# Performance work log

Hardware: AMD Instinct MI355X
Metric: run time of the kernel (lower is better)

Reference implementation:

```python
import jax, jax.numpy as jnp
import numpy as np

N_TOKENS = 4096   # flattened batch*seq tokens
D_MODEL = 1024
N_EXPERT = 8
D_HIDDEN = 1024   # expert FFN hidden size
TOP_K = 2


def setup_inputs() -> dict:
    key = jax.random.key(0)
    ks = jax.random.split(key, 4)
    f32 = jnp.float32
    return {
        "inp": jax.random.normal(ks[0], (N_TOKENS, D_MODEL), f32),
        "gate_w": jax.random.normal(ks[1], (D_MODEL, N_EXPERT), f32) * 0.02,
        "gate_b": jnp.zeros((N_EXPERT,), f32),
        "w1": jax.random.normal(ks[2], (N_EXPERT, D_MODEL, D_HIDDEN), f32) * 0.02,
        "b1": jnp.zeros((N_EXPERT, D_HIDDEN), f32),
        "w2": jax.random.normal(ks[3], (N_EXPERT, D_HIDDEN, D_MODEL), f32) * 0.02,
        "b2": jnp.zeros((N_EXPERT, D_MODEL), f32),
    }


def reference(inp, gate_w, gate_b, w1, b1, w2, b2):
    """FMoE forward: NaiveGate top-k -> dispatch -> per-expert FFN -> weighted combine.

    Math is identical to dispatch/grouped-GEMM/gather: since both top-k slots of a
    token see the same input, out[n] = sum_e coeff[n,e] * expert_e(inp[n]) where
    coeff[n,e] = sum_k softmax(top_vals)[n,k] * 1[top_idx[n,k] == e].
    """
    n_expert = gate_w.shape[-1]
    # NaiveGate: linear gate, top-k, softmax over the k selected logits
    logits = inp @ gate_w + gate_b                      # [N, E]
    top_val, top_idx = jax.lax.top_k(logits, TOP_K)     # [N, K]
    score = jax.nn.softmax(top_val, axis=-1)            # [N, K]
    # combine weights per (token, expert); top-k indices are distinct per token
    coeff = jnp.sum(
        jax.nn.one_hot(top_idx, n_expert, dtype=inp.dtype) * score[..., None],
        axis=1,
    )                                                   # [N, E]
    # expert FFN (exact-erf GeLU, matching torch.nn.functional.gelu)
    h = jax.nn.gelu(jnp.einsum('nd,edh->neh', inp, w1) + b1, approximate=False)  # [N, E, H]
    out = jnp.einsum('neh,ehd->nd', h * coeff[:, :, None], w2) + coeff @ b2      # [N, D]
    return out


if __name__ == "__main__":
    out = reference(**setup_inputs())
    print(out.shape, out.dtype)
```

## Files before the change

kernel.cpp:

```cpp
#include <hip/hip_runtime.h>
#include <math.h>

#define N_TOKENS 4096
#define D_MODEL  1024
#define N_EXPERT 8
#define D_HIDDEN 1024
#define N_POS    8192

typedef __bf16 bf16x8 __attribute__((ext_vector_type(8)));
typedef float  f32x4  __attribute__((ext_vector_type(4)));
typedef unsigned short u16x8 __attribute__((ext_vector_type(8)));

#define GLOBAL_AS __attribute__((address_space(1)))
#define LDS_AS    __attribute__((address_space(3)))

static __device__ __forceinline__ void async_ld16(const void* g, void* l) {
    __builtin_amdgcn_global_load_lds((GLOBAL_AS void*)g, (LDS_AS void*)l, 16, 0, 0);
}

static __device__ __forceinline__ unsigned short f2bf(float f) {
    unsigned int u = __builtin_bit_cast(unsigned int, f);
    u += 0x7fffu + ((u >> 16) & 1u);
    return (unsigned short)(u >> 16);
}
static __device__ __forceinline__ unsigned int pack2(float a, float b) {
    return (unsigned int)f2bf(a) | ((unsigned int)f2bf(b) << 16);
}
static __device__ __forceinline__ float bflo(unsigned int u) {
    return __builtin_bit_cast(float, u << 16);
}
static __device__ __forceinline__ float bfhi(unsigned int u) {
    return __builtin_bit_cast(float, u & 0xffff0000u);
}

__global__ __launch_bounds__(256) void convert_kernel(
    const float* __restrict__ w1, const float* __restrict__ w2,
    const float* __restrict__ inp,
    unsigned short* __restrict__ w1b, unsigned short* __restrict__ w2b,
    unsigned short* __restrict__ inp_bf, int* __restrict__ cnts)
{
    int tid = threadIdx.x;
    if (blockIdx.x == 0 && blockIdx.y == 0 && blockIdx.z == 0 && tid < 8)
        cnts[tid] = 0;
    int mat = blockIdx.z;
    int r0 = blockIdx.x * 64, c0 = blockIdx.y * 64;

    if (mat >= 16) {
        const float* src = inp + (size_t)(mat - 16) * 1048576;
        unsigned short* dst = inp_bf + (size_t)(mat - 16) * 1048576;
        #pragma unroll
        for (int i = 0; i < 4; ++i) {
            int r = (tid >> 4) + i * 16;
            float4 v = *(const float4*)(src + (size_t)(r0 + r) * 1024 + c0 + (tid & 15) * 4);
            uint2 u; u.x = pack2(v.x, v.y); u.y = pack2(v.z, v.w);
            *(uint2*)(dst + (size_t)(r0 + r) * 1024 + c0 + (tid & 15) * 4) = u;
        }
        return;
    }

    const float* src = (mat < 8) ? (w1 + (size_t)mat * 1048576)
                                 : (w2 + (size_t)(mat - 8) * 1048576);
    unsigned short* dst = (mat < 8) ? (w1b + (size_t)mat * 1048576)
                                    : (w2b + (size_t)(mat - 8) * 1048576);
    __shared__ float tile[64][68];
    #pragma unroll
    for (int i = 0; i < 4; ++i) {
        int r = (tid >> 4) + i * 16;
        float4 v = *(const float4*)(src + (size_t)(r0 + r) * 1024 + c0 + (tid & 15) * 4);
        *(float4*)&tile[r][(tid & 15) * 4] = v;
    }
    __syncthreads();
    int dr = tid >> 2;
    #pragma unroll
    for (int p = 0; p < 2; ++p) {
        int ch = (tid & 3) + p * 4;
        u16x8 o;
        #pragma unroll
        for (int j = 0; j < 8; ++j) o[j] = f2bf(tile[ch * 8 + j][dr]);
        *(u16x8*)(dst + (size_t)(c0 + dr) * 1024 + r0 + ch * 8) = o;
    }
}

__global__ __launch_bounds__(256) void gate_kernel(
    const float* __restrict__ inp, const float* __restrict__ gate_w,
    const float* __restrict__ gate_b, int* __restrict__ cnts,
    int* __restrict__ emeta, float* __restrict__ stok)
{
    __shared__ int bcnt[8], base[8];
    __shared__ int tinfo[16];
    int tid = threadIdx.x, lane = tid & 63, wave = tid >> 6;
    if (tid < 8) bcnt[tid] = 0;
    __syncthreads();

    for (int t = 0; t < 4; ++t) {
        int ti = wave * 4 + t;
        int n  = blockIdx.x * 16 + ti;
        const float* ip = inp + (size_t)n * D_MODEL;
        float acc[8] = {0.f,0.f,0.f,0.f,0.f,0.f,0.f,0.f};
        for (int d0 = lane * 4; d0 < D_MODEL; d0 += 256) {
            float4 x = *(const float4*)(ip + d0);
            #pragma unroll
            for (int j = 0; j < 4; ++j) {
                float xv = (j == 0) ? x.x : (j == 1) ? x.y : (j == 2) ? x.z : x.w;
                float4 g0 = *(const float4*)(gate_w + (d0 + j) * 8);
                float4 g1 = *(const float4*)(gate_w + (d0 + j) * 8 + 4);
                acc[0] += xv * g0.x; acc[1] += xv * g0.y;
                acc[2] += xv * g0.z; acc[3] += xv * g0.w;
                acc[4] += xv * g1.x; acc[5] += xv * g1.y;
                acc[6] += xv * g1.z; acc[7] += xv * g1.w;
            }
        }
        #pragma unroll
        for (int off = 32; off > 0; off >>= 1)
            #pragma unroll
            for (int e = 0; e < 8; ++e)
                acc[e] += __shfl_xor(acc[e], off, 64);
        #pragma unroll
        for (int e = 0; e < 8; ++e) acc[e] += gate_b[e];

        int e0 = 0; float v0 = acc[0];
        #pragma unroll
        for (int e = 1; e < 8; ++e) if (acc[e] > v0) { v0 = acc[e]; e0 = e; }
        int e1 = -1; float v1 = -1e30f;
        #pragma unroll
        for (int e = 0; e < 8; ++e) if (e != e0 && acc[e] > v1) { v1 = acc[e]; e1 = e; }
        float tv = expf(v1 - v0);
        float s0 = 1.0f / (1.0f + tv);
        float s1 = tv / (1.0f + tv);

        if (lane == 0) {
            int r0 = atomicAdd(&bcnt[e0], 1);
            int r1 = atomicAdd(&bcnt[e1], 1);
            tinfo[ti] = e0 | (e1 << 4) | (r0 << 8) | (r1 << 20);
            stok[2 * n]     = s0;
            stok[2 * n + 1] = s1;
        }
    }
    __syncthreads();
    if (tid < 8) base[tid] = atomicAdd(&cnts[tid], bcnt[tid]);
    __syncthreads();
    if (tid < 16) {
        int n = blockIdx.x * 16 + tid;
        unsigned int inf = (unsigned int)tinfo[tid];
        int e0 = inf & 15, e1 = (inf >> 4) & 15;
        int p0 = base[e0] + ((inf >> 8) & 4095);
        int p1 = base[e1] + (int)(inf >> 20);
        emeta[n] = e0 | (e1 << 4) | (p0 << 8) | (p1 << 20);
    }
}

__global__ __launch_bounds__(256) void plan_kernel(
    const int* __restrict__ cnts, const int* __restrict__ emeta,
    int* __restrict__ pos2tok)
{
    int n = blockIdx.x * 256 + threadIdx.x;
    unsigned int em = (unsigned int)emeta[n];
    int e0 = em & 15, e1 = (em >> 4) & 15;
    int p0 = (em >> 8) & 4095, p1 = (int)(em >> 20);
    int off0 = 0, off1 = 0;
    #pragma unroll
    for (int e = 0; e < 8; ++e) {
        int c = cnts[e];
        off0 += (e < e0) ? c : 0;
        off1 += (e < e1) ? c : 0;
    }
    pos2tok[off0 + p0] = n;
    pos2tok[off1 + p1] = n;
}

__global__ __launch_bounds__(256, 4) void ffn1_kernel(
    const unsigned short* __restrict__ inp_bf, const unsigned short* __restrict__ w1b,
    const float* __restrict__ b1, const int* __restrict__ cnts,
    const int* __restrict__ pos2tok, unsigned short* __restrict__ Hg)
{
    int bid = blockIdx.x;
    int e = bid & 7, nt = (bid >> 3) & 15, mt = bid >> 7;
    int off = 0, Ne = 0;
    #pragma unroll
    for (int i = 0; i < 8; ++i) {
        int c = cnts[i];
        off += (i < e) ? c : 0;
        Ne = (i == e) ? c : Ne;
    }
    int m0 = mt * 128;
    if (m0 >= Ne) return;
    int n0 = nt * 64;

    __shared__ unsigned short As[2 * 128 * 32];
    __shared__ unsigned short Bs[2 * 64 * 32];
    __shared__ int rowtok[128];

    int tid = threadIdx.x, lane = tid & 63, wave = tid >> 6;
    int lrow = lane >> 2, lchunk = lane & 3;
    int csw8 = (lchunk ^ ((lrow >> 1) & 3)) * 8;

    if (tid < 128) {
        int r = m0 + tid;
        if (r >= Ne) r = Ne - 1;
        rowtok[tid] = pos2tok[off + r];
    }
    __syncthreads();

    const unsigned short* aS0 =
        inp_bf + (size_t)rowtok[wave * 32 + lrow] * D_MODEL + csw8;
    const unsigned short* aS1 =
        inp_bf + (size_t)rowtok[wave * 32 + 16 + lrow] * D_MODEL + csw8;
    const unsigned short* bS = w1b + (size_t)e * D_MODEL * D_HIDDEN
                             + (size_t)(n0 + wave * 16 + lrow) * D_MODEL + csw8;
    unsigned short* aD0 = &As[(wave * 32) * 32];
    unsigned short* aD1 = &As[(wave * 32 + 16) * 32];
    unsigned short* bD  = &Bs[(wave * 16) * 32];

    f32x4 acc[4][2] = {};
    int wm = (wave & 1) * 64, wn = ((wave >> 1) & 1) * 32;
    int lane15 = lane & 15, quad = lane >> 4;
    int fro = (quad ^ ((lane15 >> 1) & 3)) * 8;

    for (int k0 = 0; k0 < D_MODEL; k0 += 64) {
        #pragma unroll
        for (int h = 0; h < 2; ++h) {
            int ko = k0 + h * 32;
            async_ld16(aS0 + ko, aD0 + h * 4096);
            async_ld16(aS1 + ko, aD1 + h * 4096);
            async_ld16(bS  + ko, bD  + h * 2048);
        }
        __syncthreads();
        #pragma unroll
        for (int h = 0; h < 2; ++h) {
            bf16x8 af[4], bf[2];
            #pragma unroll
            for (int t = 0; t < 4; ++t)
                af[t] = *(const bf16x8*)&As[h * 4096 + (wm + t * 16 + lane15) * 32 + fro];
            #pragma unroll
            for (int t = 0; t < 2; ++t)
                bf[t] = *(const bf16x8*)&Bs[h * 2048 + (wn + t * 16 + lane15) * 32 + fro];
            #pragma unroll
            for (int i = 0; i < 4; ++i)
                #pragma unroll
                for (int j = 0; j < 2; ++j)
                    acc[i][j] = __builtin_amdgcn_mfma_f32_16x16x32_bf16(
                        af[i], bf[j], acc[i][j], 0, 0, 0);
        }
        if (k0 + 64 < D_MODEL) __syncthreads();
    }

    const float* bexp = b1 + (size_t)e * D_HIDDEN;
    #pragma unroll
    for (int j = 0; j < 2; ++j) {
        int gcol = n0 + wn + j * 16 + lane15;
        float bv = bexp[gcol];
        #pragma unroll
        for (int i = 0; i < 4; ++i) {
            int rowb = wm + i * 16 + quad * 4;
            #pragma unroll
            for (int r = 0; r < 4; ++r) {
                int row = rowb + r;
                if (m0 + row < Ne) {
                    float x = acc[i][j][r] + bv;
                    float gv = 0.5f * x * (1.0f + erff(x * 0.70710678118654752f));
                    Hg[(size_t)(off + m0 + row) * D_HIDDEN + gcol] = f2bf(gv);
                }
            }
        }
    }
}

__global__ __launch_bounds__(256, 4) void ffn2_kernel(
    const unsigned short* __restrict__ Hg, const unsigned short* __restrict__ w2b,
    const int* __restrict__ cnts, unsigned short* __restrict__ Og)
{
    int bid = blockIdx.x;
    int e = bid & 7, nt = (bid >> 3) & 15, mt = bid >> 7;
    int off = 0, Ne = 0;
    #pragma unroll
    for (int i = 0; i < 8; ++i) {
        int c = cnts[i];
        off += (i < e) ? c : 0;
        Ne = (i == e) ? c : Ne;
    }
    int m0 = mt * 128;
    if (m0 >= Ne) return;
    int n0 = nt * 64;

    __shared__ unsigned short As[2 * 128 * 32];
    __shared__ unsigned short Bs[2 * 64 * 32];

    int tid = threadIdx.x, lane = tid & 63, wave = tid >> 6;
    int lrow = lane >> 2, lchunk = lane & 3;
    int csw8 = (lchunk ^ ((lrow >> 1) & 3)) * 8;

    int ga0 = off + m0 + wave * 32 + lrow;
    int ga1 = ga0 + 16;
    if (ga0 >= N_POS) ga0 = N_POS - 1;
    if (ga1 >= N_POS) ga1 = N_POS - 1;
    const unsigned short* aS0 = Hg + (size_t)ga0 * D_HIDDEN + csw8;
    const unsigned short* aS1 = Hg + (size_t)ga1 * D_HIDDEN + csw8;
    const unsigned short* bS = w2b + (size_t)e * D_HIDDEN * D_MODEL
                             + (size_t)(n0 + wave * 16 + lrow) * D_HIDDEN + csw8;
    unsigned short* aD0 = &As[(wave * 32) * 32];
    unsigned short* aD1 = &As[(wave * 32 + 16) * 32];
    unsigned short* bD  = &Bs[(wave * 16) * 32];

    f32x4 acc[4][2] = {};
    int wm = (wave & 1) * 64, wn = ((wave >> 1) & 1) * 32;
    int lane15 = lane & 15, quad = lane >> 4;
    int fro = (quad ^ ((lane15 >> 1) & 3)) * 8;

    for (int k0 = 0; k0 < D_HIDDEN; k0 += 64) {
        #pragma unroll
        for (int h = 0; h < 2; ++h) {
            int ko = k0 + h * 32;
            async_ld16(aS0 + ko, aD0 + h * 4096);
            async_ld16(aS1 + ko, aD1 + h * 4096);
            async_ld16(bS  + ko, bD  + h * 2048);
        }
        __syncthreads();
        #pragma unroll
        for (int h = 0; h < 2; ++h) {
            bf16x8 af[4], bf[2];
            #pragma unroll
            for (int t = 0; t < 4; ++t)
                af[t] = *(const bf16x8*)&As[h * 4096 + (wm + t * 16 + lane15) * 32 + fro];
            #pragma unroll
            for (int t = 0; t < 2; ++t)
                bf[t] = *(const bf16x8*)&Bs[h * 2048 + (wn + t * 16 + lane15) * 32 + fro];
            #pragma unroll
            for (int i = 0; i < 4; ++i)
                #pragma unroll
                for (int j = 0; j < 2; ++j)
                    acc[i][j] = __builtin_amdgcn_mfma_f32_16x16x32_bf16(
                        af[i], bf[j], acc[i][j], 0, 0, 0);
        }
        if (k0 + 64 < D_HIDDEN) __syncthreads();
    }

    #pragma unroll
    for (int j = 0; j < 2; ++j) {
        int gcol = n0 + wn + j * 16 + lane15;
        #pragma unroll
        for (int i = 0; i < 4; ++i) {
            int rowb = wm + i * 16 + quad * 4;
            #pragma unroll
            for (int r = 0; r < 4; ++r) {
                int row = rowb + r;
                if (m0 + row < Ne) {
                    Og[(size_t)(off + m0 + row) * D_MODEL + gcol] =
                        f2bf(acc[i][j][r]);
                }
            }
        }
    }
}

__global__ __launch_bounds__(256) void combine_kernel(
    const unsigned short* __restrict__ Og, const int* __restrict__ cnts,
    const int* __restrict__ emeta, const float* __restrict__ stok,
    const float* __restrict__ b2, float* __restrict__ out)
{
    int lane = threadIdx.x & 63, wave = threadIdx.x >> 6;
    int n = blockIdx.x * 4 + wave;
    unsigned int em = (unsigned int)emeta[n];
    int e0 = em & 15, e1 = (em >> 4) & 15;
    int p0 = (em >> 8) & 4095, p1 = (int)(em >> 20);
    int off0 = 0, off1 = 0;
    #pragma unroll
    for (int e = 0; e < 8; ++e) {
        int c = cnts[e];
        off0 += (e < e0) ? c : 0;
        off1 += (e < e1) ? c : 0;
    }
    int pos0 = off0 + p0, pos1 = off1 + p1;
    float s0 = stok[2 * n], s1 = stok[2 * n + 1];
    const unsigned short* o0 = Og + (size_t)pos0 * D_MODEL;
    const unsigned short* o1 = Og + (size_t)pos1 * D_MODEL;
    const float* bA = b2 + (size_t)e0 * D_MODEL;
    const float* bB = b2 + (size_t)e1 * D_MODEL;
    float* op = out + (size_t)n * D_MODEL;
    for (int d = lane * 4; d < D_MODEL; d += 256) {
        uint2 u0 = *(const uint2*)(o0 + d);
        uint2 u1 = *(const uint2*)(o1 + d);
        float4 xa = *(const float4*)(bA + d);
        float4 xb = *(const float4*)(bB + d);
        float4 r;
        r.x = s0 * (bflo(u0.x) + xa.x) + s1 * (bflo(u1.x) + xb.x);
        r.y = s0 * (bfhi(u0.x) + xa.y) + s1 * (bfhi(u1.x) + xb.y);
        r.z = s0 * (bflo(u0.y) + xa.z) + s1 * (bflo(u1.y) + xb.z);
        r.w = s0 * (bfhi(u0.y) + xa.w) + s1 * (bfhi(u1.y) + xb.w);
        *(float4*)(op + d) = r;
    }
}

extern "C" void kernel_launch(void* const* d_in, const int* in_sizes, int n_in,
                              void* d_out, int out_size, void* d_ws, size_t ws_size,
                              hipStream_t stream) {
    const float* inp    = (const float*)d_in[0];
    const float* gate_w = (const float*)d_in[1];
    const float* gate_b = (const float*)d_in[2];
    const float* w1     = (const float*)d_in[3];
    const float* b1     = (const float*)d_in[4];
    const float* w2     = (const float*)d_in[5];
    const float* b2     = (const float*)d_in[6];
    float* out = (float*)d_out;

    char* ws = (char*)d_ws;
    int*   cnts    = (int*)  (ws);
    int*   emeta   = (int*)  (ws + 4096);
    float* stok    = (float*)(ws + 65536);
    int*   pos2tok = (int*)  (ws + 131072);
    unsigned short* w2b = (unsigned short*)(ws + 1048576);
    unsigned short* Hg  = (unsigned short*)(ws + 17825792);
    unsigned short* w1b = (unsigned short*)(ws + 34603008);
    unsigned short* Og  = (unsigned short*)(ws + 34603008);

    unsigned short* inp_bf = (unsigned short*)d_out;

    convert_kernel<<<dim3(16, 16, 20), 256, 0, stream>>>(
        w1, w2, inp, w1b, w2b, inp_bf, cnts);
    gate_kernel<<<dim3(N_TOKENS / 16), 256, 0, stream>>>(
        inp, gate_w, gate_b, cnts, emeta, stok);
    plan_kernel<<<dim3(N_TOKENS / 256), 256, 0, stream>>>(cnts, emeta, pos2tok);
    ffn1_kernel<<<dim3(4096), 256, 0, stream>>>(
        inp_bf, w1b, b1, cnts, pos2tok, Hg);
    ffn2_kernel<<<dim3(4096), 256, 0, stream>>>(Hg, w2b, cnts, Og);
    combine_kernel<<<dim3(N_TOKENS / 4), 256, 0, stream>>>(
        Og, cnts, emeta, stok, b2, out);
}
```

Measured before the change: 224.5 us.

## Fuse MoE pipeline into one persistent cooperative kernel with grid syncs

Replaces the six separate launches (convert, gate, plan, ffn1, ffn2, combine) with a single cooperative kernel of 512 persistent blocks that loops over work items and separates stages with grid-wide syncs. Expert counting no longer uses global atomics: per-group counts are written out and one block computes the prefix offsets, a token-to-position map and the position-to-token map. The aim is to remove per-launch overhead and inter-kernel gaps. In exchange, occupancy is capped at two blocks per CU (down from four in the GEMM kernels), which may hurt latency hiding in the expert GEMMs, and the single-block planning step adds a serial phase.

```diff
diff --git a/kernel.cpp b/kernel.cpp
--- a/kernel.cpp
+++ b/kernel.cpp
@@ -1,5 +1,8 @@
 #include <hip/hip_runtime.h>
+#include <hip/hip_cooperative_groups.h>
 #include <math.h>
+
+namespace cg = cooperative_groups;
 
 #define N_TOKENS 4096
 #define D_MODEL  1024
@@ -33,360 +36,356 @@
     return __builtin_bit_cast(float, u & 0xffff0000u);
 }
 
-__global__ __launch_bounds__(256) void convert_kernel(
-    const float* __restrict__ w1, const float* __restrict__ w2,
-    const float* __restrict__ inp,
+__global__ __launch_bounds__(256, 2) void moe_kernel(
+    const float* __restrict__ inp, const float* __restrict__ gate_w,
+    const float* __restrict__ gate_b, const float* __restrict__ w1,
+    const float* __restrict__ b1, const float* __restrict__ w2,
+    const float* __restrict__ b2,
     unsigned short* __restrict__ w1b, unsigned short* __restrict__ w2b,
-    unsigned short* __restrict__ inp_bf, int* __restrict__ cnts)
+    unsigned short* __restrict__ inp_bf, unsigned short* __restrict__ Hg,
+    unsigned short* __restrict__ Og,
+    int* __restrict__ gcnt, int* __restrict__ emeta, float* __restrict__ stok,
+    int* __restrict__ pos2tok, int* __restrict__ tok2pos,
+    int* __restrict__ cnts, float* __restrict__ out)
 {
-    int tid = threadIdx.x;
-    if (blockIdx.x == 0 && blockIdx.y == 0 && blockIdx.z == 0 && tid < 8)
-        cnts[tid] = 0;
-    int mat = blockIdx.z;
-    int r0 = blockIdx.x * 64, c0 = blockIdx.y * 64;
-
-    if (mat >= 16) {
-        const float* src = inp + (size_t)(mat - 16) * 1048576;
-        unsigned short* dst = inp_bf + (size_t)(mat - 16) * 1048576;
-        #pragma unroll
-        for (int i = 0; i < 4; ++i) {
-            int r = (tid >> 4) + i * 16;
-            float4 v = *(const float4*)(src + (size_t)(r0 + r) * 1024 + c0 + (tid & 15) * 4);
-            uint2 u; u.x = pack2(v.x, v.y); u.y = pack2(v.z, v.w);
-            *(uint2*)(dst + (size_t)(r0 + r) * 1024 + c0 + (tid & 15) * 4) = u;
-        }
-        return;
+    cg::grid_group grid = cg::this_grid();
+    __shared__ __align__(16) char smem[25088];
+
+    int bid = blockIdx.x, tid = threadIdx.x;
+    int lane = tid & 63, wave = tid >> 6;
+    int lane15 = lane & 15, quad = lane >> 4;
+
+    for (int job = bid; job < 5376; job += 512) {
+        if (job < 5120) {
+            int mat = job >> 8, t = job & 255;
+            int r0 = (t & 15) * 64, c0 = (t >> 4) * 64;
+            if (mat >= 16) {
+                const float* src = inp + (size_t)(mat - 16) * 1048576;
+                unsigned short* dst = inp_bf + (size_t)(mat - 16) * 1048576;
+                #pragma unroll
+                for (int i = 0; i < 4; ++i) {
+                    int r = (tid >> 4) + i * 16;
+                    float4 v = *(const float4*)(src + (size_t)(r0 + r) * 1024
+                                                + c0 + (tid & 15) * 4);
+                    uint2 u; u.x = pack2(v.x, v.y); u.y = pack2(v.z, v.w);
+                    *(uint2*)(dst + (size_t)(r0 + r) * 1024 + c0 + (tid & 15) * 4) = u;
+                }
+            } else {
+                const float* src = (mat < 8) ? (w1 + (size_t)mat * 1048576)
+                                             : (w2 + (size_t)(mat - 8) * 1048576);
+                unsigned short* dst = (mat < 8) ? (w1b + (size_t)mat * 1048576)
+                                                : (w2b + (size_t)(mat - 8) * 1048576);
+                float (*tile)[68] = (float(*)[68])smem;
+                #pragma unroll
+                for (int i = 0; i < 4; ++i) {
+                    int r = (tid >> 4) + i * 16;
+                    float4 v = *(const float4*)(src + (size_t)(r0 + r) * 1024
+                                                + c0 + (tid & 15) * 4);
+                    *(float4*)&tile[r][(tid & 15) * 4] = v;
+                }
+                __syncthreads();
+                int dr = tid >> 2;
+                #pragma unroll
+                for (int p = 0; p < 2; ++p) {
+                    int ch = (tid & 3) + p * 4;
+                    u16x8 o;
+                    #pragma unroll
+                    for (int j = 0; j < 8; ++j) o[j] = f2bf(tile[ch * 8 + j][dr]);
+                    *(u16x8*)(dst + (size_t)(c0 + dr) * 1024 + r0 + ch * 8) = o;
+                }
+            }
+        } else {
+            int g = job - 5120;
+            int* bcnt  = (int*)smem;
+            int* tinfo = bcnt + 8;
+            if (tid < 8) bcnt[tid] = 0;
+            __syncthreads();
+            for (int t = 0; t < 4; ++t) {
+                int ti = wave * 4 + t;
+                int n  = g * 16 + ti;
+                const float* ip = inp + (size_t)n * D_MODEL;
+                float acc[8] = {0.f,0.f,0.f,0.f,0.f,0.f,0.f,0.f};
+                for (int d0 = lane * 4; d0 < D_MODEL; d0 += 256) {
+                    float4 x = *(const float4*)(ip + d0);
+                    #pragma unroll
+                    for (int j = 0; j < 4; ++j) {
+                        float xv = (j == 0) ? x.x : (j == 1) ? x.y
+                                 : (j == 2) ? x.z : x.w;
+                        float4 g0 = *(const float4*)(gate_w + (d0 + j) * 8);
+                        float4 g1 = *(const float4*)(gate_w + (d0 + j) * 8 + 4);
+                        acc[0] += xv * g0.x; acc[1] += xv * g0.y;
+                        acc[2] += xv * g0.z; acc[3] += xv * g0.w;
+                        acc[4] += xv * g1.x; acc[5] += xv * g1.y;
+                        acc[6] += xv * g1.z; acc[7] += xv * g1.w;
+                    }
+                }
+                #pragma unroll
+                for (int off = 32; off > 0; off >>= 1)
+                    #pragma unroll
+                    for (int e = 0; e < 8; ++e)
+                        acc[e] += __shfl_xor(acc[e], off, 64);
+                #pragma unroll
+                for (int e = 0; e < 8; ++e) acc[e] += gate_b[e];
+
+                int e0 = 0; float v0 = acc[0];
+                #pragma unroll
+                for (int e = 1; e < 8; ++e) if (acc[e] > v0) { v0 = acc[e]; e0 = e; }
+                int e1 = -1; float v1 = -1e30f;
+                #pragma unroll
+                for (int e = 0; e < 8; ++e)
+                    if (e != e0 && acc[e] > v1) { v1 = acc[e]; e1 = e; }
+                float tv = expf(v1 - v0);
+                float s0 = 1.0f / (1.0f + tv);
+                float s1 = tv / (1.0f + tv);
+                if (lane == 0) {
+                    int r0 = atomicAdd(&bcnt[e0], 1);
+                    int r1 = atomicAdd(&bcnt[e1], 1);
+                    tinfo[ti] = e0 | (e1 << 4) | (r0 << 8) | (r1 << 20);
+                    stok[2 * n]     = s0;
+                    stok[2 * n + 1] = s1;
+                }
+            }
+            __syncthreads();
+            if (tid < 8)  gcnt[g * 8 + tid]  = bcnt[tid];
+            if (tid < 16) emeta[g * 16 + tid] = tinfo[tid];
+        }
+        __syncthreads();
     }
-
-    const float* src = (mat < 8) ? (w1 + (size_t)mat * 1048576)
-                                 : (w2 + (size_t)(mat - 8) * 1048576);
-    unsigned short* dst = (mat < 8) ? (w1b + (size_t)mat * 1048576)
-                                    : (w2b + (size_t)(mat - 8) * 1048576);
-    __shared__ float tile[64][68];
-    #pragma unroll
-    for (int i = 0; i < 4; ++i) {
-        int r = (tid >> 4) + i * 16;
-        float4 v = *(const float4*)(src + (size_t)(r0 + r) * 1024 + c0 + (tid & 15) * 4);
-        *(float4*)&tile[r][(tid & 15) * 4] = v;
+    grid.sync();
+
+    if (bid == 0) {
+        int* lc  = (int*)smem;
+        int* lb  = lc + 2048;
+        int* lex = lb + 2048;
+        for (int i = tid; i < 2048; i += 256) lc[i] = gcnt[i];
+        __syncthreads();
+        if (tid < 8) {
+            int run = 0;
+            for (int g = 0; g < 256; ++g) {
+                lb[g * 8 + tid] = run;
+                run += lc[g * 8 + tid];
+            }
+            lex[8 + tid] = run;
+            cnts[tid] = run;
+        }
+        __syncthreads();
+        if (tid == 0) {
+            int o = 0;
+            #pragma unroll
+            for (int e = 0; e < 8; ++e) { lex[e] = o; o += lex[8 + e]; }
+        }
+        __syncthreads();
+        {
+            int g = tid;
+            for (int ti = 0; ti < 16; ++ti) {
+                int n = g * 16 + ti;
+                unsigned int em = (unsigned int)emeta[n];
+                int e0 = em & 15, e1 = (em >> 4) & 15;
+                int r0 = (em >> 8) & 4095, r1 = (int)(em >> 20);
+                int pos0 = lex[e0] + lb[g * 8 + e0] + r0;
+                int pos1 = lex[e1] + lb[g * 8 + e1] + r1;
+                tok2pos[2 * n]     = pos0;
+                tok2pos[2 * n + 1] = pos1;
+                pos2tok[pos0] = n;
+                pos2tok[pos1] = n;
+            }
+        }
     }
-    __syncthreads();
-    int dr = tid >> 2;
-    #pragma unroll
-    for (int p = 0; p < 2; ++p) {
-        int ch = (tid & 3) + p * 4;
-        u16x8 o;
-        #pragma unroll
-        for (int j = 0; j < 8; ++j) o[j] = f2bf(tile[ch * 8 + j][dr]);
-        *(u16x8*)(dst + (size_t)(c0 + dr) * 1024 + r0 + ch * 8) = o;
-    }
-}
-
-__global__ __launch_bounds__(256) void gate_kernel(
-    const float* __restrict__ inp, const float* __restrict__ gate_w,
-    const float* __restrict__ gate_b, int* __restrict__ cnts,
-    int* __restrict__ emeta, float* __restrict__ stok)
-{
-    __shared__ int bcnt[8], base[8];
-    __shared__ int tinfo[16];
-    int tid = threadIdx.x, lane = tid & 63, wave = tid >> 6;
-    if (tid < 8) bcnt[tid] = 0;
-    __syncthreads();
-
-    for (int t = 0; t < 4; ++t) {
-        int ti = wave * 4 + t;
-        int n  = blockIdx.x * 16 + ti;
-        const float* ip = inp + (size_t)n * D_MODEL;
-        float acc[8] = {0.f,0.f,0.f,0.f,0.f,0.f,0.f,0.f};
-        for (int d0 = lane * 4; d0 < D_MODEL; d0 += 256) {
-            float4 x = *(const float4*)(ip + d0);
-            #pragma unroll
-            for (int j = 0; j < 4; ++j) {
-                float xv = (j == 0) ? x.x : (j == 1) ? x.y : (j == 2) ? x.z : x.w;
-                float4 g0 = *(const float4*)(gate_w + (d0 + j) * 8);
-                float4 g1 = *(const float4*)(gate_w + (d0 + j) * 8 + 4);
-                acc[0] += xv * g0.x; acc[1] += xv * g0.y;
-                acc[2] += xv * g0.z; acc[3] += xv * g0.w;
-                acc[4] += xv * g1.x; acc[5] += xv * g1.y;
-                acc[6] += xv * g1.z; acc[7] += xv * g1.w;
-            }
-        }
-        #pragma unroll
-        for (int off = 32; off > 0; off >>= 1)
-            #pragma unroll
-            for (int e = 0; e < 8; ++e)
-                acc[e] += __shfl_xor(acc[e], off, 64);
-        #pragma unroll
-        for (int e = 0; e < 8; ++e) acc[e] += gate_b[e];
-
-        int e0 = 0; float v0 = acc[0];
-        #pragma unroll
-        for (int e = 1; e < 8; ++e) if (acc[e] > v0) { v0 = acc[e]; e0 = e; }
-        int e1 = -1; float v1 = -1e30f;
-        #pragma unroll
-        for (int e = 0; e < 8; ++e) if (e != e0 && acc[e] > v1) { v1 = acc[e]; e1 = e; }
-        float tv = expf(v1 - v0);
-        float s0 = 1.0f / (1.0f + tv);
-        float s1 = tv / (1.0f + tv);
-
-        if (lane == 0) {
-            int r0 = atomicAdd(&bcnt[e0], 1);
-            int r1 = atomicAdd(&bcnt[e1], 1);
-            tinfo[ti] = e0 | (e1 << 4) | (r0 << 8) | (r1 << 20);
-            stok[2 * n]     = s0;
-            stok[2 * n + 1] = s1;
-        }
-    }
-    __syncthreads();
-    if (tid < 8) base[tid] = atomicAdd(&cnts[tid], bcnt[tid]);
-    __syncthreads();
-    if (tid < 16) {
-        int n = blockIdx.x * 16 + tid;
-        unsigned int inf = (unsigned int)tinfo[tid];
-        int e0 = inf & 15, e1 = (inf >> 4) & 15;
-        int p0 = base[e0] + ((inf >> 8) & 4095);
-        int p1 = base[e1] + (int)(inf >> 20);
-        emeta[n] = e0 | (e1 << 4) | (p0 << 8) | (p1 << 20);
-    }
-}
-
-__global__ __launch_bounds__(256) void plan_kernel(
-    const int* __restrict__ cnts, const int* __restrict__ emeta,
-    int* __restrict__ pos2tok)
-{
-    int n = blockIdx.x * 256 + threadIdx.x;
-    unsigned int em = (unsigned int)emeta[n];
-    int e0 = em & 15, e1 = (em >> 4) & 15;
-    int p0 = (em >> 8) & 4095, p1 = (int)(em >> 20);
-    int off0 = 0, off1 = 0;
-    #pragma unroll
-    for (int e = 0; e < 8; ++e) {
-        int c = cnts[e];
-        off0 += (e < e0) ? c : 0;
-        off1 += (e < e1) ? c : 0;
-    }
-    pos2tok[off0 + p0] = n;
-    pos2tok[off1 + p1] = n;
-}
-
-__global__ __launch_bounds__(256, 4) void ffn1_kernel(
-    const unsigned short* __restrict__ inp_bf, const unsigned short* __restrict__ w1b,
-    const float* __restrict__ b1, const int* __restrict__ cnts,
-    const int* __restrict__ pos2tok, unsigned short* __restrict__ Hg)
-{
-    int bid = blockIdx.x;
-    int e = bid & 7, nt = (bid >> 3) & 15, mt = bid >> 7;
-    int off = 0, Ne = 0;
-    #pragma unroll
-    for (int i = 0; i < 8; ++i) {
-        int c = cnts[i];
-        off += (i < e) ? c : 0;
-        Ne = (i == e) ? c : Ne;
-    }
-    int m0 = mt * 128;
-    if (m0 >= Ne) return;
-    int n0 = nt * 64;
-
-    __shared__ unsigned short As[2 * 128 * 32];
-    __shared__ unsigned short Bs[2 * 64 * 32];
-    __shared__ int rowtok[128];
-
-    int tid = threadIdx.x, lane = tid & 63, wave = tid >> 6;
+    grid.sync();
+
+    unsigned short* As = (unsigned short*)smem;
+    unsigned short* Bs = As + 8192;
+    int* rowtok = (int*)(Bs + 4096);
+
     int lrow = lane >> 2, lchunk = lane & 3;
     int csw8 = (lchunk ^ ((lrow >> 1) & 3)) * 8;
-
-    if (tid < 128) {
-        int r = m0 + tid;
-        if (r >= Ne) r = Ne - 1;
-        rowtok[tid] = pos2tok[off + r];
+    int wm = (wave & 1) * 64, wn = ((wave >> 1) & 1) * 32;
+    int fro = (quad ^ ((lane15 >> 1) & 3)) * 8;
+
+    for (int job = bid; job < 4096; job += 512) {
+        int e = job & 7, nt = (job >> 3) & 15, mt = job >> 7;
+        int off = 0, Ne = 0;
+        #pragma unroll
+        for (int i = 0; i < 8; ++i) {
+            int c = cnts[i];
+            off += (i < e) ? c : 0;
+            Ne = (i == e) ? c : Ne;
+        }
+        int m0 = mt * 128;
+        if (m0 >= Ne) continue;
+        int n0 = nt * 64;
+        __syncthreads();
+
+        if (tid < 128) {
+            int r = m0 + tid;
+            if (r >= Ne) r = Ne - 1;
+            rowtok[tid] = pos2tok[off + r];
+        }
+        __syncthreads();
+
+        const unsigned short* aS0 =
+            inp_bf + (size_t)rowtok[wave * 32 + lrow] * D_MODEL + csw8;
+        const unsigned short* aS1 =
+            inp_bf + (size_t)rowtok[wave * 32 + 16 + lrow] * D_MODEL + csw8;
+        const unsigned short* bS = w1b + (size_t)e * D_MODEL * D_HIDDEN
+                                 + (size_t)(n0 + wave * 16 + lrow) * D_MODEL + csw8;
+        unsigned short* aD0 = &As[(wave * 32) * 32];
+        unsigned short* aD1 = &As[(wave * 32 + 16) * 32];
+        unsigned short* bD  = &Bs[(wave * 16) * 32];
+
+        f32x4 acc[4][2] = {};
+        for (int k0 = 0; k0 < D_MODEL; k0 += 64) {
+            #pragma unroll
+            for (int h = 0; h < 2; ++h) {
+                int ko = k0 + h * 32;
+                async_ld16(aS0 + ko, aD0 + h * 4096);
+                async_ld16(aS1 + ko, aD1 + h * 4096);
+                async_ld16(bS  + ko, bD  + h * 2048);
+            }
+            __syncthreads();
+            #pragma unroll
+            for (int h = 0; h < 2; ++h) {
+                bf16x8 af[4], bf[2];
+                #pragma unroll
+                for (int t = 0; t < 4; ++t)
+                    af[t] = *(const bf16x8*)
+                        &As[h * 4096 + (wm + t * 16 + lane15) * 32 + fro];
+                #pragma unroll
+                for (int t = 0; t < 2; ++t)
+                    bf[t] = *(const bf16x8*)
+                        &Bs[h * 2048 + (wn + t * 16 + lane15) * 32 + fro];
+                #pragma unroll
+                for (int i = 0; i < 4; ++i)
+                    #pragma unroll
+                    for (int j = 0; j < 2; ++j)
+                        acc[i][j] = __builtin_amdgcn_mfma_f32_16x16x32_bf16(
+                            af[i], bf[j], acc[i][j], 0, 0, 0);
+            }
+            if (k0 + 64 < D_MODEL) __syncthreads();
+        }
+
+        const float* bexp = b1 + (size_t)e * D_HIDDEN;
+        #pragma unroll
+        for (int j = 0; j < 2; ++j) {
+            int gcol = n0 + wn + j * 16 + lane15;
+            float bv = bexp[gcol];
+            #pragma unroll
+            for (int i = 0; i < 4; ++i) {
+                int rowb = wm + i * 16 + quad * 4;
+                #pragma unroll
+                for (int r = 0; r < 4; ++r) {
+                    int row = rowb + r;
+                    if (m0 + row < Ne) {
+                        float x = acc[i][j][r] + bv;
+                        float gv = 0.5f * x *
+                            (1.0f + erff(x * 0.70710678118654752f));
+                        Hg[(size_t)(off + m0 + row) * D_HIDDEN + gcol] = f2bf(gv);
+                    }
+                }
+            }
+        }
     }
-    __syncthreads();
-
-    const unsigned short* aS0 =
-        inp_bf + (size_t)rowtok[wave * 32 + lrow] * D_MODEL + csw8;
-    const unsigned short* aS1 =
-        inp_bf + (size_t)rowtok[wave * 32 + 16 + lrow] * D_MODEL + csw8;
-    const unsigned short* bS = w1b + (size_t)e * D_MODEL * D_HIDDEN
-                             + (size_t)(n0 + wave * 16 + lrow) * D_MODEL + csw8;
-    unsigned short* aD0 = &As[(wave * 32) * 32];
-    unsigned short* aD1 = &As[(wave * 32 + 16) * 32];
-    unsigned short* bD  = &Bs[(wave * 16) * 32];
-
-    f32x4 acc[4][2] = {};
-    int wm = (wave & 1) * 64, wn = ((wave >> 1) & 1) * 32;
-    int lane15 = lane & 15, quad = lane >> 4;
-    int fro = (quad ^ ((lane15 >> 1) & 3)) * 8;
-
-    for (int k0 = 0; k0 < D_MODEL; k0 += 64) {
+    grid.sync();
+
+    for (int job = bid; job < 4096; job += 512) {
+        int e = job & 7, nt = (job >> 3) & 15, mt = job >> 7;
+        int off = 0, Ne = 0;
         #pragma unroll
-        for (int h = 0; h < 2; ++h) {
-            int ko = k0 + h * 32;
-            async_ld16(aS0 + ko, aD0 + h * 4096);
-            async_ld16(aS1 + ko, aD1 + h * 4096);
-            async_ld16(bS  + ko, bD  + h * 2048);
-        }
-        __syncthreads();
+        for (int i = 0; i < 8; ++i) {
+            int c = cnts[i];
+            off += (i < e) ? c : 0;
+            Ne = (i == e) ? c : Ne;
+        }
+        int m0 = mt * 128;
+        if (m0 >= Ne) continue;
+        int n0 = nt * 64;
+        __syncthreads();
+
+        int ga0 = off + m0 + wave * 32 + lrow;
+        int ga1 = ga0 + 16;
+        if (ga0 >= N_POS) ga0 = N_POS - 1;
+        if (ga1 >= N_POS) ga1 = N_POS - 1;
+        const unsigned short* aS0 = Hg + (size_t)ga0 * D_HIDDEN + csw8;
+        const unsigned short* aS1 = Hg + (size_t)ga1 * D_HIDDEN + csw8;
+        const unsigned short* bS = w2b + (size_t)e * D_HIDDEN * D_MODEL
+                                 + (size_t)(n0 + wave * 16 + lrow) * D_HIDDEN + csw8;
+        unsigned short* aD0 = &As[(wave * 32) * 32];
+        unsigned short* aD1 = &As[(wave * 32 + 16) * 32];
+        unsigned short* bD  = &Bs[(wave * 16) * 32];
+
+        f32x4 acc[4][2] = {};
+        for (int k0 = 0; k0 < D_HIDDEN; k0 += 64) {
+            #pragma unroll
+            for (int h = 0; h < 2; ++h) {
+                int ko = k0 + h * 32;
+                async_ld16(aS0 + ko, aD0 + h * 4096);
+                async_ld16(aS1 + ko, aD1 + h * 4096);
+                async_ld16(bS  + ko, bD  + h * 2048);
+            }
+            __syncthreads();
+            #pragma unroll
+            for (int h = 0; h < 2; ++h) {
+                bf16x8 af[4], bf[2];
+                #pragma unroll
+                for (int t = 0; t < 4; ++t)
+                    af[t] = *(const bf16x8*)
+                        &As[h * 4096 + (wm + t * 16 + lane15) * 32 + fro];
+                #pragma unroll
+                for (int t = 0; t < 2; ++t)
+                    bf[t] = *(const bf16x8*)
+                        &Bs[h * 2048 + (wn + t * 16 + lane15) * 32 + fro];
+                #pragma unroll
+                for (int i = 0; i < 4; ++i)
+                    #pragma unroll
+                    for (int j = 0; j < 2; ++j)
+                        acc[i][j] = __builtin_amdgcn_mfma_f32_16x16x32_bf16(
+                            af[i], bf[j], acc[i][j], 0, 0, 0);
+            }
+            if (k0 + 64 < D_HIDDEN) __syncthreads();
+        }
+
         #pragma unroll
-        for (int h = 0; h < 2; ++h) {
-            bf16x8 af[4], bf[2];
-            #pragma unroll
-            for (int t = 0; t < 4; ++t)
-                af[t] = *(const bf16x8*)&As[h * 4096 + (wm + t * 16 + lane15) * 32 + fro];
-            #pragma unroll
-            for (int t = 0; t < 2; ++t)
-                bf[t] = *(const bf16x8*)&Bs[h * 2048 + (wn + t * 16 + lane15) * 32 + fro];
-            #pragma unroll
-            for (int i = 0; i < 4; ++i)
-                #pragma unroll
-                for (int j = 0; j < 2; ++j)
-                    acc[i][j] = __builtin_amdgcn_mfma_f32_16x16x32_bf16(
-                        af[i], bf[j], acc[i][j], 0, 0, 0);
-        }
-        if (k0 + 64 < D_MODEL) __syncthreads();
+        for (int j = 0; j < 2; ++j) {
+            int gcol = n0 + wn + j * 16 + lane15;
+            #pragma unroll
+            for (int i = 0; i < 4; ++i) {
+                int rowb = wm + i * 16 + quad * 4;
+                #pragma unroll
+                for (int r = 0; r < 4; ++r) {
+                    int row = rowb + r;
+                    if (m0 + row < Ne) {
+                        Og[(size_t)(off + m0 + row) * D_MODEL + gcol] =
+                            f2bf(acc[i][j][r]);
+                    }
+                }
+            }
+        }
     }
-
-    const float* bexp = b1 + (size_t)e * D_HIDDEN;
-    #pragma unroll
-    for (int j = 0; j < 2; ++j) {
-        int gcol = n0 + wn + j * 16 + lane15;
-        float bv = bexp[gcol];
-        #pragma unroll
-        for (int i = 0; i < 4; ++i) {
-            int rowb = wm + i * 16 + quad * 4;
-            #pragma unroll
-            for (int r = 0; r < 4; ++r) {
-                int row = rowb + r;
-                if (m0 + row < Ne) {
-                    float x = acc[i][j][r] + bv;
-                    float gv = 0.5f * x * (1.0f + erff(x * 0.70710678118654752f));
-                    Hg[(size_t)(off + m0 + row) * D_HIDDEN + gcol] = f2bf(gv);
-                }
-            }
-        }
-    }
-}
-
-__global__ __launch_bounds__(256, 4) void ffn2_kernel(
-    const unsigned short* __restrict__ Hg, const unsigned short* __restrict__ w2b,
-    const int* __restrict__ cnts, unsigned short* __restrict__ Og)
-{
-    int bid = blockIdx.x;
-    int e = bid & 7, nt = (bid >> 3) & 15, mt = bid >> 7;
-    int off = 0, Ne = 0;
-    #pragma unroll
-    for (int i = 0; i < 8; ++i) {
-        int c = cnts[i];
-        off += (i < e) ? c : 0;
-        Ne = (i == e) ? c : Ne;
-    }
-    int m0 = mt * 128;
-    if (m0 >= Ne) return;
-    int n0 = nt * 64;
-
-    __shared__ unsigned short As[2 * 128 * 32];
-    __shared__ unsigned short Bs[2 * 64 * 32];
-
-    int tid = threadIdx.x, lane = tid & 63, wave = tid >> 6;
-    int lrow = lane >> 2, lchunk = lane & 3;
-    int csw8 = (lchunk ^ ((lrow >> 1) & 3)) * 8;
-
-    int ga0 = off + m0 + wave * 32 + lrow;
-    int ga1 = ga0 + 16;
-    if (ga0 >= N_POS) ga0 = N_POS - 1;
-    if (ga1 >= N_POS) ga1 = N_POS - 1;
-    const unsigned short* aS0 = Hg + (size_t)ga0 * D_HIDDEN + csw8;
-    const unsigned short* aS1 = Hg + (size_t)ga1 * D_HIDDEN + csw8;
-    const unsigned short* bS = w2b + (size_t)e * D_HIDDEN * D_MODEL
-                             + (size_t)(n0 + wave * 16 + lrow) * D_HIDDEN + csw8;
-    unsigned short* aD0 = &As[(wave * 32) * 32];
-    unsigned short* aD1 = &As[(wave * 32 + 16) * 32];
-    unsigned short* bD  = &Bs[(wave * 16) * 32];
-
-    f32x4 acc[4][2] = {};
-    int wm = (wave & 1) * 64, wn = ((wave >> 1) & 1) * 32;
-    int lane15 = lane & 15, quad = lane >> 4;
-    int fro = (quad ^ ((lane15 >> 1) & 3)) * 8;
-
-    for (int k0 = 0; k0 < D_HIDDEN; k0 += 64) {
-        #pragma unroll
-        for (int h = 0; h < 2; ++h) {
-            int ko = k0 + h * 32;
-            async_ld16(aS0 + ko, aD0 + h * 4096);
-            async_ld16(aS1 + ko, aD1 + h * 4096);
-            async_ld16(bS  + ko, bD  + h * 2048);
-        }
-        __syncthreads();
-        #pragma unroll
-        for (int h = 0; h < 2; ++h) {
-            bf16x8 af[4], bf[2];
-            #pragma unroll
-            for (int t = 0; t < 4; ++t)
-                af[t] = *(const bf16x8*)&As[h * 4096 + (wm + t * 16 + lane15) * 32 + fro];
-            #pragma unroll
-            for (int t = 0; t < 2; ++t)
-                bf[t] = *(const bf16x8*)&Bs[h * 2048 + (wn + t * 16 + lane15) * 32 + fro];
-            #pragma unroll
-            for (int i = 0; i < 4; ++i)
-                #pragma unroll
-                for (int j = 0; j < 2; ++j)
-                    acc[i][j] = __builtin_amdgcn_mfma_f32_16x16x32_bf16(
-                        af[i], bf[j], acc[i][j], 0, 0, 0);
-        }
-        if (k0 + 64 < D_HIDDEN) __syncthreads();
-    }
-
-    #pragma unroll
-    for (int j = 0; j < 2; ++j) {
-        int gcol = n0 + wn + j * 16 + lane15;
-        #pragma unroll
-        for (int i = 0; i < 4; ++i) {
-            int rowb = wm + i * 16 + quad * 4;
-            #pragma unroll
-            for (int r = 0; r < 4; ++r) {
-                int row = rowb + r;
-                if (m0 + row < Ne) {
-                    Og[(size_t)(off + m0 + row) * D_MODEL + gcol] =
-                        f2bf(acc[i][j][r]);
-                }
-            }
-        }
-    }
-}
-
-__global__ __launch_bounds__(256) void combine_kernel(
-    const unsigned short* __restrict__ Og, const int* __restrict__ cnts,
-    const int* __restrict__ emeta, const float* __restrict__ stok,
-    const float* __restrict__ b2, float* __restrict__ out)
-{
-    int lane = threadIdx.x & 63, wave = threadIdx.x >> 6;
-    int n = blockIdx.x * 4 + wave;
-    unsigned int em = (unsigned int)emeta[n];
-    int e0 = em & 15, e1 = (em >> 4) & 15;
-    int p0 = (em >> 8) & 4095, p1 = (int)(em >> 20);
-    int off0 = 0, off1 = 0;
-    #pragma unroll
-    for (int e = 0; e < 8; ++e) {
-        int c = cnts[e];
-        off0 += (e < e0) ? c : 0;
-        off1 += (e < e1) ? c : 0;
-    }
-    int pos0 = off0 + p0, pos1 = off1 + p1;
-    float s0 = stok[2 * n], s1 = stok[2 * n + 1];
-    const unsigned short* o0 = Og + (size_t)pos0 * D_MODEL;
-    const unsigned short* o1 = Og + (size_t)pos1 * D_MODEL;
-    const float* bA = b2 + (size_t)e0 * D_MODEL;
-    const float* bB = b2 + (size_t)e1 * D_MODEL;
-    float* op = out + (size_t)n * D_MODEL;
-    for (int d = lane * 4; d < D_MODEL; d += 256) {
-        uint2 u0 = *(const uint2*)(o0 + d);
-        uint2 u1 = *(const uint2*)(o1 + d);
-        float4 xa = *(const float4*)(bA + d);
-        float4 xb = *(const float4*)(bB + d);
-        float4 r;
-        r.x = s0 * (bflo(u0.x) + xa.x) + s1 * (bflo(u1.x) + xb.x);
-        r.y = s0 * (bfhi(u0.x) + xa.y) + s1 * (bfhi(u1.x) + xb.y);
-        r.z = s0 * (bflo(u0.y) + xa.z) + s1 * (bflo(u1.y) + xb.z);
-        r.w = s0 * (bfhi(u0.y) + xa.w) + s1 * (bfhi(u1.y) + xb.w);
-        *(float4*)(op + d) = r;
+    grid.sync();
+
+    for (int job = bid; job < 1024; job += 512) {
+        int n = job * 4 + wave;
+        int pos0 = tok2pos[2 * n], pos1 = tok2pos[2 * n + 1];
+        unsigned int em = (unsigned int)emeta[n];
+        int e0 = em & 15, e1 = (em >> 4) & 15;
+        float s0 = stok[2 * n], s1 = stok[2 * n + 1];
+        const unsigned short* o0 = Og + (size_t)pos0 * D_MODEL;
+        const unsigned short* o1 = Og + (size_t)pos1 * D_MODEL;
+        const float* bA = b2 + (size_t)e0 * D_MODEL;
+        const float* bB = b2 + (size_t)e1 * D_MODEL;
+        float* op = out + (size_t)n * D_MODEL;
+        for (int d = lane * 4; d < D_MODEL; d += 256) {
+            uint2 u0 = *(const uint2*)(o0 + d);
+            uint2 u1 = *(const uint2*)(o1 + d);
+            float4 xa = *(const float4*)(bA + d);
+            float4 xb = *(const float4*)(bB + d);
+            float4 r;
+            r.x = s0 * (bflo(u0.x) + xa.x) + s1 * (bflo(u1.x) + xb.x);
+            r.y = s0 * (bfhi(u0.x) + xa.y) + s1 * (bfhi(u1.x) + xb.y);
+            r.z = s0 * (bflo(u0.y) + xa.z) + s1 * (bflo(u1.y) + xb.z);
+            r.w = s0 * (bfhi(u0.y) + xa.w) + s1 * (bfhi(u1.y) + xb.w);
+            *(float4*)(op + d) = r;
+        }
     }
 }
 
@@ -407,21 +406,19 @@
     int*   emeta   = (int*)  (ws + 4096);
     float* stok    = (float*)(ws + 65536);
     int*   pos2tok = (int*)  (ws + 131072);
+    int*   tok2pos = (int*)  (ws + 196608);
+    int*   gcnt    = (int*)  (ws + 262144);
     unsigned short* w2b = (unsigned short*)(ws + 1048576);
     unsigned short* Hg  = (unsigned short*)(ws + 17825792);
     unsigned short* w1b = (unsigned short*)(ws + 34603008);
     unsigned short* Og  = (unsigned short*)(ws + 34603008);
-
     unsigned short* inp_bf = (unsigned short*)d_out;
-
-    convert_kernel<<<dim3(16, 16, 20), 256, 0, stream>>>(
-        w1, w2, inp, w1b, w2b, inp_bf, cnts);
-    gate_kernel<<<dim3(N_TOKENS / 16), 256, 0, stream>>>(
-        inp, gate_w, gate_b, cnts, emeta, stok);
-    plan_kernel<<<dim3(N_TOKENS / 256), 256, 0, stream>>>(cnts, emeta, pos2tok);
-    ffn1_kernel<<<dim3(4096), 256, 0, stream>>>(
-        inp_bf, w1b, b1, cnts, pos2tok, Hg);
-    ffn2_kernel<<<dim3(4096), 256, 0, stream>>>(Hg, w2b, cnts, Og);
-    combine_kernel<<<dim3(N_TOKENS / 4), 256, 0, stream>>>(
-        Og, cnts, emeta, stok, b2, out);
-}
+    void* args[] = {
+        (void*)&inp, (void*)&gate_w, (void*)&gate_b, (void*)&w1, (void*)&b1,
+        (void*)&w2, (void*)&b2, (void*)&w1b, (void*)&w2b, (void*)&inp_bf,
+        (void*)&Hg, (void*)&Og, (void*)&gcnt, (void*)&emeta, (void*)&stok,
+        (void*)&pos2tok, (void*)&tok2pos, (void*)&cnts, (void*)&out,
+    };
+    hipLaunchCooperativeKernel((const void*)moe_kernel, dim3(512), dim3(256),
+                               args, 0, stream);
+}
```

Result: slower. 473.5 us (+110.9%).
